# Optimization experiments

Measured on AMD Instinct MI355X. Metric: run time of the kernel, lower is better.

Reference implementation:

```python
import jax, jax.numpy as jnp
import numpy as np

N = 4096

def setup_inputs() -> dict:
    key = jax.random.key(0)
    k1, k2, k3 = jax.random.split(key, 3)
    x = jax.random.normal(k1, (N, N), dtype=jnp.float32)
    # nn.Linear(N, N, bias=False) weight matrices, shape [out, in] = [N, N]
    s = 1.0 / np.sqrt(N)
    W_r = jax.random.uniform(k2, (N, N), dtype=jnp.float32, minval=-s, maxval=s)
    W_i = jax.random.uniform(k3, (N, N), dtype=jnp.float32, minval=-s, maxval=s)
    return {"x": x, "W_r": W_r, "W_i": W_i}

def reference(x, W_r, W_i):
    # Row pass: fft_in_rows[i] = Linear_real(x[i]) + 1j * Linear_imag(x[i])
    #   => R = x @ W_r^T + 1j * (x @ W_i^T)
    R_r = x @ W_r.T            # [N, N]
    R_i = x @ W_i.T            # [N, N]
    # Column pass: fft_in_cols[:, i] = fft_in_rows[:, i] @ (W_r + 1j W_i)
    #   => C = W^T @ R with W = W_r + 1j W_i (complex matmul in real arithmetic)
    C_r = W_r.T @ R_r - W_i.T @ R_i
    C_i = W_r.T @ R_i + W_i.T @ R_r
    # res = cat([real, imag], dim=1) -> [N, 2N]
    return jnp.concatenate([C_r, C_i], axis=1)
```

## Files before the change

kernel.cpp:

```cpp
#include <hip/hip_runtime.h>
#include <hip/hip_bf16.h>

#define NN 4096

typedef unsigned short u16;
using bf16x8 = __attribute__((ext_vector_type(8))) short;
using f32x4  = __attribute__((ext_vector_type(4))) float;
using u32x4  = __attribute__((ext_vector_type(4))) unsigned int;

__device__ inline u16 f2bf(float f) {
    union { float f; unsigned u; } c; c.f = f;
    unsigned r = (c.u + 0x7fffu + ((c.u >> 16) & 1u)) >> 16;
    return (u16)r;
}

__device__ inline void gld16(const void* g, void* l) {
    __builtin_amdgcn_global_load_lds(
        (const __attribute__((address_space(1))) void*)g,
        (__attribute__((address_space(3))) void*)l, 16, 0, 0);
}

__device__ inline bf16x8 negbf(bf16x8 v) {
    u32x4 u; __builtin_memcpy(&u, &v, 16);
    u ^= 0x80008000u;
    bf16x8 r; __builtin_memcpy(&r, &u, 16);
    return r;
}

__device__ inline void swz_tile(int bid, int& brow, int& bcol) {
    const int xcd   = bid & 7;
    const int local = bid >> 3;
    const int rr    = xcd >> 1;
    const int rc    = xcd & 1;
    brow = (rr * 8  + (local >> 4)) * 128;
    bcol = (rc * 16 + (local & 15)) * 128;
}

__global__ __launch_bounds__(256) void cvt_bf16(const float* __restrict__ s,
                                                u16* __restrict__ d) {
    size_t i = ((size_t)blockIdx.x * 256 + threadIdx.x) * 8;
    float4 v0 = *(const float4*)(s + i);
    float4 v1 = *(const float4*)(s + i + 4);
    bf16x8 o;
    o[0] = (short)f2bf(v0.x); o[1] = (short)f2bf(v0.y);
    o[2] = (short)f2bf(v0.z); o[3] = (short)f2bf(v0.w);
    o[4] = (short)f2bf(v1.x); o[5] = (short)f2bf(v1.y);
    o[6] = (short)f2bf(v1.z); o[7] = (short)f2bf(v1.w);
    *(bf16x8*)(d + i) = o;
}

__global__ __launch_bounds__(256) void tr_cvt(const float* __restrict__ s,
                                              u16* __restrict__ d) {
    __shared__ float t[32][33];
    int x  = blockIdx.x * 32 + threadIdx.x;
    int y0 = blockIdx.y * 32;
#pragma unroll
    for (int j = 0; j < 32; j += 8)
        t[threadIdx.y + j][threadIdx.x] = s[(size_t)(y0 + threadIdx.y + j) * NN + x];
    __syncthreads();
    int x2 = blockIdx.y * 32 + threadIdx.x;
    int y2 = blockIdx.x * 32;
#pragma unroll
    for (int j = 0; j < 32; j += 8)
        d[(size_t)(y2 + threadIdx.y + j) * NN + x2] = f2bf(t[threadIdx.x][threadIdx.y + j]);
}


__global__ __launch_bounds__(256, 2) void gemm_pass1(
    const u16* __restrict__ Ar, const u16* __restrict__ Ai,
    const u16* __restrict__ B,
    u16* __restrict__ Cr, u16* __restrict__ Ci) {
    __shared__ u16 sm[2][3][4096];

    int brow, bcol;
    swz_tile(blockIdx.x, brow, bcol);

    const int tid  = threadIdx.x;
    const int lane = tid & 63;
    const int wid  = tid >> 6;
    const int wm   = (wid >> 1) * 64;
    const int wn   = (wid & 1) * 64;

    f32x4 accr[4][4] = {};
    f32x4 acci[4][4] = {};

    const int r0 = tid >> 2;
    const int lb = (tid & 3) ^ ((r0 >> 1) & 3);
    const size_t aoff0 = (size_t)(brow + r0) * NN + lb * 8;
    const size_t aoff1 = aoff0 + (size_t)64 * NN;
    const size_t boff0 = (size_t)(bcol + r0) * NN + lb * 8;
    const size_t boff1 = boff0 + (size_t)64 * NN;
    const int rl = lane & 15;
    const int kg = ((lane >> 4) ^ ((rl >> 1) & 3)) * 8;

#define STG1(buf, kk) do { \
    gld16(Ar + aoff0 + (kk), &sm[buf][0][tid * 8]); \
    gld16(Ar + aoff1 + (kk), &sm[buf][0][2048 + tid * 8]); \
    gld16(Ai + aoff0 + (kk), &sm[buf][1][tid * 8]); \
    gld16(Ai + aoff1 + (kk), &sm[buf][1][2048 + tid * 8]); \
    gld16(B  + boff0 + (kk), &sm[buf][2][tid * 8]); \
    gld16(B  + boff1 + (kk), &sm[buf][2][2048 + tid * 8]); \
} while (0)

    auto compute = [&](int buf) {
        bf16x8 ar[4], ai[4], b[4];
#pragma unroll
        for (int i = 0; i < 4; i++) {
            ar[i] = *(const bf16x8*)&sm[buf][0][(wm + i * 16 + rl) * 32 + kg];
            ai[i] = *(const bf16x8*)&sm[buf][1][(wm + i * 16 + rl) * 32 + kg];
        }
#pragma unroll
        for (int j = 0; j < 4; j++)
            b[j] = *(const bf16x8*)&sm[buf][2][(wn + j * 16 + rl) * 32 + kg];
#pragma unroll
        for (int i = 0; i < 4; i++)
#pragma unroll
            for (int j = 0; j < 4; j++) {
                accr[i][j] = __builtin_amdgcn_mfma_f32_16x16x32_bf16(ar[i], b[j], accr[i][j], 0, 0, 0);
                acci[i][j] = __builtin_amdgcn_mfma_f32_16x16x32_bf16(ai[i], b[j], acci[i][j], 0, 0, 0);
            }
    };

    STG1(0, 0);
    __syncthreads();
    int cur = 0;
    for (int t = 0; t < NN / 32 - 1; t++) {
        STG1(cur ^ 1, (t + 1) * 32);
        compute(cur);
        __syncthreads();
        cur ^= 1;
    }
    compute(cur);

    const int rg = (lane >> 4) * 4;
#pragma unroll
    for (int i = 0; i < 4; i++)
#pragma unroll
        for (int j = 0; j < 4; j++) {
            int col = bcol + wn + j * 16 + rl;
#pragma unroll
            for (int r = 0; r < 4; r++) {
                int row = brow + wm + i * 16 + rg + r;
                Cr[(size_t)row * NN + col] = f2bf(accr[i][j][r]);
                Ci[(size_t)row * NN + col] = f2bf(acci[i][j][r]);
            }
        }
#undef STG1
}

__global__ __launch_bounds__(256, 2) void gemm_pass2(
    const u16* __restrict__ Ar, const u16* __restrict__ Ai,
    const u16* __restrict__ Br, const u16* __restrict__ Bi,
    float* __restrict__ Out) {
    __shared__ u16 sm[2][4][4096];

    int brow, bcol;
    swz_tile(blockIdx.x, brow, bcol);

    const int tid  = threadIdx.x;
    const int lane = tid & 63;
    const int wid  = tid >> 6;
    const int wm   = (wid >> 1) * 64;
    const int wn   = (wid & 1) * 64;

    f32x4 accr[4][4] = {};
    f32x4 acci[4][4] = {};

    const int r0 = tid >> 2;
    const int lb = (tid & 3) ^ ((r0 >> 1) & 3);
    const size_t moff0 = (size_t)(brow + r0) * NN + lb * 8;
    const size_t moff1 = moff0 + (size_t)64 * NN;
    const size_t noff0 = (size_t)(bcol + r0) * NN + lb * 8;
    const size_t noff1 = noff0 + (size_t)64 * NN;
    const int rl = lane & 15;
    const int kg = ((lane >> 4) ^ ((rl >> 1) & 3)) * 8;

#define STAGE2(buf, kk) do { \
    gld16(Ar + moff0 + (kk), &sm[buf][0][tid * 8]); \
    gld16(Ar + moff1 + (kk), &sm[buf][0][2048 + tid * 8]); \
    gld16(Ai + moff0 + (kk), &sm[buf][1][tid * 8]); \
    gld16(Ai + moff1 + (kk), &sm[buf][1][2048 + tid * 8]); \
    gld16(Br + noff0 + (kk), &sm[buf][2][tid * 8]); \
    gld16(Br + noff1 + (kk), &sm[buf][2][2048 + tid * 8]); \
    gld16(Bi + noff0 + (kk), &sm[buf][3][tid * 8]); \
    gld16(Bi + noff1 + (kk), &sm[buf][3][2048 + tid * 8]); \
} while (0)

    auto compute = [&](int buf) {
        bf16x8 ar[4], ai[4], br[4], bi[4];
#pragma unroll
        for (int i = 0; i < 4; i++) {
            ar[i] = *(const bf16x8*)&sm[buf][0][(wm + i * 16 + rl) * 32 + kg];
            ai[i] = *(const bf16x8*)&sm[buf][1][(wm + i * 16 + rl) * 32 + kg];
        }
#pragma unroll
        for (int j = 0; j < 4; j++) {
            br[j] = *(const bf16x8*)&sm[buf][2][(wn + j * 16 + rl) * 32 + kg];
            bi[j] = *(const bf16x8*)&sm[buf][3][(wn + j * 16 + rl) * 32 + kg];
        }
#pragma unroll
        for (int i = 0; i < 4; i++)
#pragma unroll
            for (int j = 0; j < 4; j++) {
                acci[i][j] = __builtin_amdgcn_mfma_f32_16x16x32_bf16(ar[i], bi[j], acci[i][j], 0, 0, 0);
                acci[i][j] = __builtin_amdgcn_mfma_f32_16x16x32_bf16(ai[i], br[j], acci[i][j], 0, 0, 0);
            }
#pragma unroll
        for (int i = 0; i < 4; i++) ai[i] = negbf(ai[i]);
#pragma unroll
        for (int i = 0; i < 4; i++)
#pragma unroll
            for (int j = 0; j < 4; j++) {
                accr[i][j] = __builtin_amdgcn_mfma_f32_16x16x32_bf16(ar[i], br[j], accr[i][j], 0, 0, 0);
                accr[i][j] = __builtin_amdgcn_mfma_f32_16x16x32_bf16(ai[i], bi[j], accr[i][j], 0, 0, 0);
            }
    };

    STAGE2(0, 0);
    __syncthreads();
    int cur = 0;
    for (int t = 0; t < NN / 32 - 1; t++) {
        STAGE2(cur ^ 1, (t + 1) * 32);
        compute(cur);
        __syncthreads();
        cur ^= 1;
    }
    compute(cur);

    const int rg = (lane >> 4) * 4;
#pragma unroll
    for (int i = 0; i < 4; i++)
#pragma unroll
        for (int j = 0; j < 4; j++) {
            int col = bcol + wn + j * 16 + rl;
#pragma unroll
            for (int r = 0; r < 4; r++) {
                int row = brow + wm + i * 16 + rg + r;
                Out[(size_t)row * (2 * NN) + col]      = accr[i][j][r];
                Out[(size_t)row * (2 * NN) + NN + col] = acci[i][j][r];
            }
        }
#undef STAGE2
}

extern "C" void kernel_launch(void* const* d_in, const int* in_sizes, int n_in,
                              void* d_out, int out_size, void* d_ws, size_t ws_size,
                              hipStream_t stream) {
    const float* x  = (const float*)d_in[0];
    const float* Wr = (const float*)d_in[1];
    const float* Wi = (const float*)d_in[2];
    float* out = (float*)d_out;

    const size_t SZ = (size_t)NN * NN;
    u16* ws  = (u16*)d_ws;
    u16* xb  = ws;
    u16* Wrb = ws + SZ;
    u16* Wib = ws + 2 * SZ;
    u16* Rtr = ws + 3 * SZ;
    u16* Rti = ws + 4 * SZ;

    cvt_bf16<<<8192, 256, 0, stream>>>(x,  xb);
    cvt_bf16<<<8192, 256, 0, stream>>>(Wr, Wrb);
    cvt_bf16<<<8192, 256, 0, stream>>>(Wi, Wib);

    gemm_pass1<<<1024, 256, 0, stream>>>(Wrb, Wib, xb, Rtr, Rti);

    u16* WrT = xb;
    u16* WiT = Wrb;
    tr_cvt<<<dim3(128, 128), dim3(32, 8), 0, stream>>>(Wr, WrT);
    tr_cvt<<<dim3(128, 128), dim3(32, 8), 0, stream>>>(Wi, WiT);

    gemm_pass2<<<1024, 256, 0, stream>>>(WrT, WiT, Rtr, Rti, out);
}
```

Baseline: 786.5 us.

## Interleave LDS reads, global prefetch and MFMA chains with barriers and setprio

Both GEMM passes replace the monolithic read-then-compute loop body with a phased schedule. Each phase reads a subset of fragments from LDS, issues part of the next tile's global-to-LDS loads, synchronises with explicit barriers and lgkmcnt waits, then runs one 16-MFMA chain at raised wave priority. The aim is to spread memory issue across the MFMA work, cut register pressure from holding all fragments at once, and coordinate waves in a ping-pong fashion. The cost is several extra block barriers per k-step, which could stall waves. The last iteration's hardcoded buffer index of 1 relies on the iteration count being even.

```diff
diff --git a/kernel.cpp b/kernel.cpp
--- a/kernel.cpp
+++ b/kernel.cpp
@@ -65,6 +65,28 @@
         d[(size_t)(y2 + threadIdx.y + j) * NN + x2] = f2bf(t[threadIdx.x][threadIdx.y + j]);
 }
 
+#define P_BAR  __builtin_amdgcn_s_barrier()
+#define P_LGKM do { asm volatile("s_waitcnt lgkmcnt(0)" ::: "memory"); \
+                    __builtin_amdgcn_sched_barrier(0); } while (0)
+#define P_VM0  do { asm volatile("s_waitcnt vmcnt(0)" ::: "memory"); \
+                    __builtin_amdgcn_sched_barrier(0); } while (0)
+
+#define CHAIN(AF, BF, ACC) do { \
+    __builtin_amdgcn_s_setprio(1); \
+    _Pragma("unroll") \
+    for (int i_ = 0; i_ < 4; i_++) \
+        _Pragma("unroll") \
+        for (int j_ = 0; j_ < 4; j_++) \
+            ACC[i_][j_] = __builtin_amdgcn_mfma_f32_16x16x32_bf16(AF[i_], BF[j_], ACC[i_][j_], 0, 0, 0); \
+    __builtin_amdgcn_s_setprio(0); \
+} while (0)
+
+#define RD4(DST, CC, TILE, BASE) do { \
+    _Pragma("unroll") \
+    for (int i_ = 0; i_ < 4; i_++) \
+        DST[i_] = *(const bf16x8*)&sm[CC][TILE][((BASE) + i_ * 16 + rl) * 32 + kg]; \
+} while (0)
+
 
 __global__ __launch_bounds__(256, 2) void gemm_pass1(
     const u16* __restrict__ Ar, const u16* __restrict__ Ai,
@@ -93,44 +115,36 @@
     const int rl = lane & 15;
     const int kg = ((lane >> 4) ^ ((rl >> 1) & 3)) * 8;
 
-#define STG1(buf, kk) do { \
-    gld16(Ar + aoff0 + (kk), &sm[buf][0][tid * 8]); \
-    gld16(Ar + aoff1 + (kk), &sm[buf][0][2048 + tid * 8]); \
-    gld16(Ai + aoff0 + (kk), &sm[buf][1][tid * 8]); \
-    gld16(Ai + aoff1 + (kk), &sm[buf][1][2048 + tid * 8]); \
-    gld16(B  + boff0 + (kk), &sm[buf][2][tid * 8]); \
-    gld16(B  + boff1 + (kk), &sm[buf][2][2048 + tid * 8]); \
-} while (0)
-
-    auto compute = [&](int buf) {
-        bf16x8 ar[4], ai[4], b[4];
-#pragma unroll
-        for (int i = 0; i < 4; i++) {
-            ar[i] = *(const bf16x8*)&sm[buf][0][(wm + i * 16 + rl) * 32 + kg];
-            ai[i] = *(const bf16x8*)&sm[buf][1][(wm + i * 16 + rl) * 32 + kg];
-        }
-#pragma unroll
-        for (int j = 0; j < 4; j++)
-            b[j] = *(const bf16x8*)&sm[buf][2][(wn + j * 16 + rl) * 32 + kg];
-#pragma unroll
-        for (int i = 0; i < 4; i++)
-#pragma unroll
-            for (int j = 0; j < 4; j++) {
-                accr[i][j] = __builtin_amdgcn_mfma_f32_16x16x32_bf16(ar[i], b[j], accr[i][j], 0, 0, 0);
-                acci[i][j] = __builtin_amdgcn_mfma_f32_16x16x32_bf16(ai[i], b[j], acci[i][j], 0, 0, 0);
-            }
-    };
-
-    STG1(0, 0);
-    __syncthreads();
-    int cur = 0;
-    for (int t = 0; t < NN / 32 - 1; t++) {
-        STG1(cur ^ 1, (t + 1) * 32);
-        compute(cur);
-        __syncthreads();
-        cur ^= 1;
+#define T0(b, kk) gld16(Ar + aoff0 + (kk), &sm[b][0][tid * 8])
+#define T1(b, kk) gld16(Ar + aoff1 + (kk), &sm[b][0][2048 + tid * 8])
+#define T2(b, kk) gld16(Ai + aoff0 + (kk), &sm[b][1][tid * 8])
+#define T3(b, kk) gld16(Ai + aoff1 + (kk), &sm[b][1][2048 + tid * 8])
+#define T4(b, kk) gld16(B  + boff0 + (kk), &sm[b][2][tid * 8])
+#define T5(b, kk) gld16(B  + boff1 + (kk), &sm[b][2][2048 + tid * 8])
+
+#define KSTEP1(CC, NB, KN, DOSTG) do { \
+    bf16x8 af[4], ag[4], bb[4]; \
+    RD4(af, CC, 0, wm); RD4(bb, CC, 2, wn); \
+    if (DOSTG) { T0(NB, KN); T1(NB, KN); T2(NB, KN); T3(NB, KN); } \
+    P_BAR; P_LGKM; \
+    CHAIN(af, bb, accr); \
+    P_BAR; \
+    RD4(ag, CC, 1, wm); \
+    if (DOSTG) { T4(NB, KN); T5(NB, KN); } \
+    P_BAR; P_LGKM; \
+    CHAIN(ag, bb, acci); \
+    if (DOSTG) P_VM0; \
+    P_BAR; \
+} while (0)
+
+    T0(0, 0); T1(0, 0); T2(0, 0); T3(0, 0); T4(0, 0); T5(0, 0);
+    P_VM0;
+    P_BAR;
+    for (int t = 0; t < NN / 32 - 1; ++t) {
+        const int cc = t & 1, nb = cc ^ 1;
+        KSTEP1(cc, nb, (size_t)(t + 1) * 32, 1);
     }
-    compute(cur);
+    KSTEP1(1, 0, 0, 0);
 
     const int rg = (lane >> 4) * 4;
 #pragma unroll
@@ -145,7 +159,6 @@
                 Ci[(size_t)row * NN + col] = f2bf(acci[i][j][r]);
             }
         }
-#undef STG1
 }
 
 __global__ __launch_bounds__(256, 2) void gemm_pass2(
@@ -175,57 +188,51 @@
     const int rl = lane & 15;
     const int kg = ((lane >> 4) ^ ((rl >> 1) & 3)) * 8;
 
-#define STAGE2(buf, kk) do { \
-    gld16(Ar + moff0 + (kk), &sm[buf][0][tid * 8]); \
-    gld16(Ar + moff1 + (kk), &sm[buf][0][2048 + tid * 8]); \
-    gld16(Ai + moff0 + (kk), &sm[buf][1][tid * 8]); \
-    gld16(Ai + moff1 + (kk), &sm[buf][1][2048 + tid * 8]); \
-    gld16(Br + noff0 + (kk), &sm[buf][2][tid * 8]); \
-    gld16(Br + noff1 + (kk), &sm[buf][2][2048 + tid * 8]); \
-    gld16(Bi + noff0 + (kk), &sm[buf][3][tid * 8]); \
-    gld16(Bi + noff1 + (kk), &sm[buf][3][2048 + tid * 8]); \
-} while (0)
-
-    auto compute = [&](int buf) {
-        bf16x8 ar[4], ai[4], br[4], bi[4];
-#pragma unroll
-        for (int i = 0; i < 4; i++) {
-            ar[i] = *(const bf16x8*)&sm[buf][0][(wm + i * 16 + rl) * 32 + kg];
-            ai[i] = *(const bf16x8*)&sm[buf][1][(wm + i * 16 + rl) * 32 + kg];
-        }
-#pragma unroll
-        for (int j = 0; j < 4; j++) {
-            br[j] = *(const bf16x8*)&sm[buf][2][(wn + j * 16 + rl) * 32 + kg];
-            bi[j] = *(const bf16x8*)&sm[buf][3][(wn + j * 16 + rl) * 32 + kg];
-        }
-#pragma unroll
-        for (int i = 0; i < 4; i++)
-#pragma unroll
-            for (int j = 0; j < 4; j++) {
-                acci[i][j] = __builtin_amdgcn_mfma_f32_16x16x32_bf16(ar[i], bi[j], acci[i][j], 0, 0, 0);
-                acci[i][j] = __builtin_amdgcn_mfma_f32_16x16x32_bf16(ai[i], br[j], acci[i][j], 0, 0, 0);
-            }
-#pragma unroll
-        for (int i = 0; i < 4; i++) ai[i] = negbf(ai[i]);
-#pragma unroll
-        for (int i = 0; i < 4; i++)
-#pragma unroll
-            for (int j = 0; j < 4; j++) {
-                accr[i][j] = __builtin_amdgcn_mfma_f32_16x16x32_bf16(ar[i], br[j], accr[i][j], 0, 0, 0);
-                accr[i][j] = __builtin_amdgcn_mfma_f32_16x16x32_bf16(ai[i], bi[j], accr[i][j], 0, 0, 0);
-            }
-    };
-
-    STAGE2(0, 0);
-    __syncthreads();
-    int cur = 0;
-    for (int t = 0; t < NN / 32 - 1; t++) {
-        STAGE2(cur ^ 1, (t + 1) * 32);
-        compute(cur);
-        __syncthreads();
-        cur ^= 1;
+#define SL0(b, kk) gld16(Ar + moff0 + (kk), &sm[b][0][tid * 8])
+#define SL1(b, kk) gld16(Ar + moff1 + (kk), &sm[b][0][2048 + tid * 8])
+#define SL2(b, kk) gld16(Ai + moff0 + (kk), &sm[b][1][tid * 8])
+#define SL3(b, kk) gld16(Ai + moff1 + (kk), &sm[b][1][2048 + tid * 8])
+#define SL4(b, kk) gld16(Br + noff0 + (kk), &sm[b][2][tid * 8])
+#define SL5(b, kk) gld16(Br + noff1 + (kk), &sm[b][2][2048 + tid * 8])
+#define SL6(b, kk) gld16(Bi + noff0 + (kk), &sm[b][3][tid * 8])
+#define SL7(b, kk) gld16(Bi + noff1 + (kk), &sm[b][3][2048 + tid * 8])
+
+#define KSTEP2(CC, NB, KN, DOSTG) do { \
+    bf16x8 ar[4], ai[4], br[4], bi[4]; \
+     \
+    RD4(ar, CC, 0, wm); RD4(bi, CC, 3, wn); \
+    if (DOSTG) { SL0(NB, KN); SL1(NB, KN); SL2(NB, KN); } \
+    P_BAR; P_LGKM; \
+    CHAIN(ar, bi, acci); \
+    P_BAR; \
+     \
+    RD4(br, CC, 2, wn); \
+    if (DOSTG) { SL3(NB, KN); SL4(NB, KN); SL5(NB, KN); } \
+    P_BAR; P_LGKM; \
+    CHAIN(ar, br, accr); \
+    P_BAR; \
+     \
+    RD4(ai, CC, 1, wm); \
+    if (DOSTG) { SL6(NB, KN); SL7(NB, KN); } \
+    P_BAR; P_LGKM; \
+    CHAIN(ai, br, acci); \
+    P_BAR; \
+     \
+    _Pragma("unroll") for (int i_ = 0; i_ < 4; i_++) ai[i_] = negbf(ai[i_]); \
+    CHAIN(ai, bi, accr); \
+    if (DOSTG) P_VM0; \
+    P_BAR; \
+} while (0)
+
+    SL0(0, 0); SL1(0, 0); SL2(0, 0); SL3(0, 0);
+    SL4(0, 0); SL5(0, 0); SL6(0, 0); SL7(0, 0);
+    P_VM0;
+    P_BAR;
+    for (int t = 0; t < NN / 32 - 1; ++t) {
+        const int cc = t & 1, nb = cc ^ 1;
+        KSTEP2(cc, nb, (size_t)(t + 1) * 32, 1);
     }
-    compute(cur);
+    KSTEP2(1, 0, 0, 0);
 
     const int rg = (lane >> 4) * 4;
 #pragma unroll
@@ -240,7 +247,6 @@
                 Out[(size_t)row * (2 * NN) + NN + col] = acci[i][j][r];
             }
         }
-#undef STAGE2
 }
 
 extern "C" void kernel_launch(void* const* d_in, const int* in_sizes, int n_in,
```

Result: faster. 770.3 us (-2.1%).
